# Kernel optimization log

Measured on AMD Instinct MI355X. Metric: run time of the kernel, lower is better.

## Reference

```python
import jax, jax.numpy as jnp
import numpy as np

B, S, DIM_IN, DIM_K, DIM_V = 4, 2048, 512, 2048, 64


def setup_inputs() -> dict:
    key = jax.random.key(0)
    k1, k2, k3, k4 = jax.random.split(key, 4)
    x = jax.random.normal(k1, (B, S, DIM_IN), dtype=jnp.float32)
    # nn.Linear(dim_in, d, bias=False) -> stored transposed here so y = x @ W
    Wq = jax.random.normal(k2, (DIM_IN, DIM_K), dtype=jnp.float32) / np.sqrt(DIM_IN)
    Wk = jax.random.normal(k3, (DIM_IN, DIM_K), dtype=jnp.float32) / np.sqrt(DIM_IN)
    Wv = jax.random.normal(k4, (DIM_IN, DIM_V), dtype=jnp.float32) / np.sqrt(DIM_IN)
    return {"x": x, "Wq": Wq, "Wk": Wk, "Wv": Wv}


def reference(x, Wq, Wk, Wv):
    dim_k = Wq.shape[-1]
    q = x @ Wq            # [B, S, dim_k]
    k = x @ Wk            # [B, S, dim_k]
    v = x @ Wv            # [B, S, dim_v]
    scores = jnp.einsum("bqd,bkd->bqk", q, k)  # [B, S, S]
    # causal mask: disallow attending to strictly-future positions
    seq = scores.shape[-1]
    mask = jnp.triu(jnp.ones((seq, seq), dtype=bool), k=1)
    scores = jnp.where(mask[None, :, :], -jnp.inf, scores)
    attn = jax.nn.softmax(scores / np.sqrt(dim_k).astype(np.float32), axis=-1)
    return attn @ v       # [B, S, dim_v]
```

## Files before the change

### kernel.cpp

```cpp
#include <hip/hip_runtime.h>
#include <hip/hip_bf16.h>
#include <math.h>

using bf16 = __hip_bfloat16;
typedef __bf16 bf16x8 __attribute__((ext_vector_type(8)));
typedef float floatx4 __attribute__((ext_vector_type(4)));

constexpr int BB = 4, SS = 2048, DIN = 512, DKK = 2048, DVV = 64;
constexpr int ROWS = BB * SS;
constexpr int LDY = 640;

constexpr size_t XB_OFF  = 0;
constexpr size_t WQB_OFF = XB_OFF  + 8388608;
constexpr size_t WKB_OFF = WQB_OFF + 2097152;
constexpr size_t WT2_OFF = WKB_OFF + 2097152;
constexpr size_t MTP_OFF = WT2_OFF + 655360;
constexpr size_t YV_OFF  = MTP_OFF + 8388608;
constexpr size_t VT_OFF  = YV_OFF  + 10485760;
constexpr size_t PRT_OFF = VT_OFF  + 1048576;
constexpr size_t STA_OFF = PRT_OFF + 16777216;

__device__ __forceinline__ void async_copy16(const bf16* g, const unsigned short* l) {
    __builtin_amdgcn_global_load_lds((const __attribute__((address_space(1))) void*)g,
                                     (__attribute__((address_space(3))) void*)l, 16, 0, 0);
}

__global__ __launch_bounds__(256) void prep(const float* __restrict__ x,
                                            const float* __restrict__ Wq,
                                            const float* __restrict__ Wk,
                                            const float* __restrict__ Wv,
                                            bf16* __restrict__ xb,
                                            bf16* __restrict__ wqb,
                                            bf16* __restrict__ wkb,
                                            bf16* __restrict__ wt2) {
    __shared__ float tile[32][33];
    const int bid = blockIdx.x;
    const int tid = threadIdx.x;

    if (bid < 4096) {
        int i = bid * 256 + tid;
        float4 v = reinterpret_cast<const float4*>(x)[i];
        union { bf16 h[4]; ushort4 u; } cv;
        cv.h[0] = __float2bfloat16(v.x);
        cv.h[1] = __float2bfloat16(v.y);
        cv.h[2] = __float2bfloat16(v.z);
        cv.h[3] = __float2bfloat16(v.w);
        reinterpret_cast<ushort4*>(xb)[i] = cv.u;
    } else if (bid < 6144) {
        int i = (bid - 4096) * 256 + tid;
        const float* src = (i < 262144) ? Wq : Wk;
        bf16* dst = (i < 262144) ? wqb : wkb;
        int j = (i < 262144) ? i : i - 262144;
        float4 v = reinterpret_cast<const float4*>(src)[j];
        union { bf16 h[4]; ushort4 u; } cv;
        cv.h[0] = __float2bfloat16(v.x);
        cv.h[1] = __float2bfloat16(v.y);
        cv.h[2] = __float2bfloat16(v.z);
        cv.h[3] = __float2bfloat16(v.w);
        reinterpret_cast<ushort4*>(dst)[j] = cv.u;
    } else {
        int idx = bid - 6144;
        int n0 = (idx & 1) * 32;
        int k0 = (idx >> 1) * 32;
        int nn = tid & 31, kk8 = tid >> 5;
        #pragma unroll
        for (int p = 0; p < 4; ++p) {
            int k = p * 8 + kk8;
            tile[k][nn] = Wv[(long long)(k0 + k) * 64 + n0 + nn];
        }
        __syncthreads();
        int kk = tid & 31, nn8 = tid >> 5;
        #pragma unroll
        for (int p = 0; p < 4; ++p) {
            int n = p * 8 + nn8;
            wt2[(long long)(512 + n0 + n) * 512 + k0 + kk] = __float2bfloat16(tile[kk][n]);
        }
    }
}

__global__ __launch_bounds__(256) void gemm_mt(const bf16* __restrict__ A,
                                               const bf16* __restrict__ Bt,
                                               float* __restrict__ Cp) {
    __shared__ __align__(16) unsigned short As[128 * 64];
    __shared__ __align__(16) unsigned short Bs[128 * 64];

    const int tid = threadIdx.x;
    const int lane = tid & 63, wave = tid >> 6;

    const int wg = (blockIdx.x & 7) * 16 + (blockIdx.x >> 3);
    const int z = wg >> 4;
    const int tile = wg & 15;
    const long long m0 = (long long)(tile >> 2) * 128;
    const long long n0 = (long long)(tile & 3) * 128;
    const int koff = z * 256;

    const int rIn = lane >> 3;
    const int cSwz = ((lane & 7) ^ rIn) * 8;
    const int wm0 = (wave >> 1) * 64, wn0 = (wave & 1) * 64;
    const int l15 = lane & 15, quad = lane >> 4;
    const int sw7 = l15 & 7;

    floatx4 acc[4][4] = {};

    for (int k0 = koff; k0 < koff + 256; k0 += 64) {
        #pragma unroll
        for (int t0 = 0; t0 < 8; ++t0) {
            int t = t0 * 4 + wave;
            if (t < 16)
                async_copy16(A + (m0 + t * 8 + rIn) * 2048LL + k0 + cSwz, &As[t * 512]);
            else
                async_copy16(Bt + (n0 + (t - 16) * 8 + rIn) * 2048LL + k0 + cSwz, &Bs[(t - 16) * 512]);
        }
        __syncthreads();
        #pragma unroll
        for (int sk = 0; sk < 2; ++sk) {
            const int rchunk = (((sk << 2) | quad) ^ sw7) * 8;
            bf16x8 af[4], bfr[4];
            #pragma unroll
            for (int mi = 0; mi < 4; ++mi)
                af[mi] = *reinterpret_cast<const bf16x8*>(&As[(wm0 + mi * 16 + l15) * 64 + rchunk]);
            #pragma unroll
            for (int ni = 0; ni < 4; ++ni)
                bfr[ni] = *reinterpret_cast<const bf16x8*>(&Bs[(wn0 + ni * 16 + l15) * 64 + rchunk]);
            #pragma unroll
            for (int mi = 0; mi < 4; ++mi)
                #pragma unroll
                for (int ni = 0; ni < 4; ++ni)
                    acc[mi][ni] = __builtin_amdgcn_mfma_f32_16x16x32_bf16(af[mi], bfr[ni],
                                                                          acc[mi][ni], 0, 0, 0);
        }
        __syncthreads();
    }

    float* C = Cp + (long long)z * 262144;
    #pragma unroll
    for (int mi = 0; mi < 4; ++mi) {
        long long row0 = m0 + wm0 + mi * 16 + quad * 4;
        #pragma unroll
        for (int ni = 0; ni < 4; ++ni) {
            long long col = n0 + wn0 + ni * 16 + l15;
            #pragma unroll
            for (int r = 0; r < 4; ++r)
                C[(row0 + r) * 512 + col] = acc[mi][ni][r];
        }
    }
}

__global__ __launch_bounds__(256) void reduce_mt(const float4* __restrict__ part,
                                                 bf16* __restrict__ wt2) {
    int i = blockIdx.x * 256 + threadIdx.x;
    float4 s = {0.f, 0.f, 0.f, 0.f};
    #pragma unroll
    for (int t = 0; t < 8; ++t) {
        float4 a = part[(long long)t * 65536 + i];
        s.x += a.x; s.y += a.y; s.z += a.z; s.w += a.w;
    }
    union { bf16 h[4]; ushort4 u; } cv;
    cv.h[0] = __float2bfloat16(s.x);
    cv.h[1] = __float2bfloat16(s.y);
    cv.h[2] = __float2bfloat16(s.z);
    cv.h[3] = __float2bfloat16(s.w);
    reinterpret_cast<ushort4*>(wt2)[i] = cv.u;
}

__global__ __launch_bounds__(256) void gemm_proj(const bf16* __restrict__ A,
                                                 const bf16* __restrict__ Bt,
                                                 bf16* __restrict__ C,
                                                 bf16* __restrict__ vt) {
    __shared__ __align__(16) unsigned short As[128 * 64];
    __shared__ __align__(16) unsigned short Bs[128 * 64];

    const int tid = threadIdx.x;
    const int lane = tid & 63, wave = tid >> 6;

    const int wg = (blockIdx.x & 7) * 40 + (blockIdx.x >> 3);
    const long long m0 = (long long)(wg / 5) * 128;
    const long long n0 = (long long)(wg % 5) * 128;

    const int rIn = lane >> 3;
    const int cSwz = ((lane & 7) ^ rIn) * 8;
    const int wm0 = (wave >> 1) * 64, wn0 = (wave & 1) * 64;
    const int l15 = lane & 15, quad = lane >> 4;
    const int sw7 = l15 & 7;

    floatx4 acc[4][4] = {};

    for (int k0 = 0; k0 < DIN; k0 += 64) {
        #pragma unroll
        for (int t0 = 0; t0 < 8; ++t0) {
            int t = t0 * 4 + wave;
            if (t < 16)
                async_copy16(A + (m0 + t * 8 + rIn) * (long long)DIN + k0 + cSwz, &As[t * 512]);
            else
                async_copy16(Bt + (n0 + (t - 16) * 8 + rIn) * (long long)DIN + k0 + cSwz, &Bs[(t - 16) * 512]);
        }
        __syncthreads();
        #pragma unroll
        for (int sk = 0; sk < 2; ++sk) {
            const int rchunk = (((sk << 2) | quad) ^ sw7) * 8;
            bf16x8 af[4], bfr[4];
            #pragma unroll
            for (int mi = 0; mi < 4; ++mi)
                af[mi] = *reinterpret_cast<const bf16x8*>(&As[(wm0 + mi * 16 + l15) * 64 + rchunk]);
            #pragma unroll
            for (int ni = 0; ni < 4; ++ni)
                bfr[ni] = *reinterpret_cast<const bf16x8*>(&Bs[(wn0 + ni * 16 + l15) * 64 + rchunk]);
            #pragma unroll
            for (int mi = 0; mi < 4; ++mi)
                #pragma unroll
                for (int ni = 0; ni < 4; ++ni)
                    acc[mi][ni] = __builtin_amdgcn_mfma_f32_16x16x32_bf16(af[mi], bfr[ni],
                                                                          acc[mi][ni], 0, 0, 0);
        }
        __syncthreads();
    }

    if (n0 < 512) {
        #pragma unroll
        for (int mi = 0; mi < 4; ++mi) {
            long long row0 = m0 + wm0 + mi * 16 + quad * 4;
            #pragma unroll
            for (int ni = 0; ni < 4; ++ni) {
                long long col = n0 + wn0 + ni * 16 + l15;
                #pragma unroll
                for (int r = 0; r < 4; ++r)
                    C[(row0 + r) * (long long)LDY + col] = __float2bfloat16(acc[mi][ni][r]);
            }
        }
    } else if (!(wave & 1)) {
        const int b = (int)(m0 >> 11);
        const int sbase = ((int)m0 & 2047) + wm0;
        #pragma unroll
        for (int mi = 0; mi < 4; ++mi) {
            int s0 = sbase + mi * 16 + quad * 4;
            #pragma unroll
            for (int ni = 0; ni < 4; ++ni) {
                int j = ni * 16 + l15;
                union { bf16 h[4]; ushort4 u; } cv;
                #pragma unroll
                for (int r = 0; r < 4; ++r)
                    cv.h[r] = __float2bfloat16(acc[mi][ni][r]);
                *reinterpret_cast<ushort4*>(vt + ((long long)(b * DVV + j)) * SS + s0) = cv.u;
            }
        }
    }
}

__global__ __launch_bounds__(512) void attn_fused(const bf16* __restrict__ yv,
                                                  const bf16* __restrict__ xb,
                                                  const bf16* __restrict__ vt,
                                                  bf16* __restrict__ part,
                                                  float* __restrict__ stats) {
    constexpr int BK = 64;
    constexpr float SCALE = 0.022097086912079608f;

    __shared__ __align__(16) char smem[37888];
    unsigned short* As = (unsigned short*)smem;
    unsigned short* Bs = (unsigned short*)(smem + 16384);
    unsigned short* Ps = (unsigned short*)smem;
    unsigned short* Vs = (unsigned short*)(smem + 18432);
    float* smax = (float*)(smem + 35840);
    float* ssum = (float*)(smem + 36864);

    const int wg = (blockIdx.x & 7) * 17 + (blockIdx.x >> 3);
    int by = (int)((sqrtf(8.f * (float)wg + 1.f) - 1.f) * 0.5f);
    while ((by + 1) * (by + 2) / 2 <= wg) ++by;
    while (by * (by + 1) / 2 > wg) --by;
    const int bx = wg - by * (by + 1) / 2;
    const int b = blockIdx.z;

    const bf16* A  = yv + (long long)b * SS * LDY;
    const bf16* Bt = xb + (long long)b * SS * 512;

    const int tid = threadIdx.x;
    const int lane = tid & 63, wave = tid >> 6;
    const long long m0 = (long long)by * 128;
    const long long n0 = (long long)bx * 128;

    const int rIn = lane >> 3;
    const int cSwz = ((lane & 7) ^ rIn) * 8;
    const int wm0 = (wave >> 1) * 32, wn0 = (wave & 1) * 64;
    const int l15 = lane & 15, quad = lane >> 4;
    const int sw7 = l15 & 7;

    floatx4 acc[2][4] = {};

    uint4 vreg[2];
    #pragma unroll
    for (int p = 0; p < 2; ++p) {
        int j = (tid >> 4) + p * 32;
        int ch = tid & 15;
        vreg[p] = *reinterpret_cast<const uint4*>(
            vt + ((long long)b * DVV + j) * SS + n0 + ch * 8);
    }

    auto issue = [&](int k0) {
        #pragma unroll
        for (int t0 = 0; t0 < 4; ++t0) {
            int t = t0 * 8 + wave;
            if (t < 16)
                async_copy16(A + (m0 + t * 8 + rIn) * (long long)LDY + k0 + cSwz,
                             &As[t * 512]);
            else
                async_copy16(Bt + (n0 + (t - 16) * 8 + rIn) * 512LL + k0 + cSwz,
                             &Bs[(t - 16) * 512]);
        }
    };

    for (int it = 0; it < DIN / BK; ++it) {
        issue(it * BK);
        __syncthreads();
        __builtin_amdgcn_s_setprio(1);
        #pragma unroll
        for (int sk = 0; sk < 2; ++sk) {
            const int rchunk = ((sk << 2) | quad) ^ sw7;
            bf16x8 af[2], bfr[4];
            #pragma unroll
            for (int mi = 0; mi < 2; ++mi)
                af[mi] = *reinterpret_cast<const bf16x8*>(
                    &As[(wm0 + mi * 16 + l15) * BK + rchunk * 8]);
            #pragma unroll
            for (int ni = 0; ni < 4; ++ni)
                bfr[ni] = *reinterpret_cast<const bf16x8*>(
                    &Bs[(wn0 + ni * 16 + l15) * BK + rchunk * 8]);
            #pragma unroll
            for (int mi = 0; mi < 2; ++mi)
                #pragma unroll
                for (int ni = 0; ni < 4; ++ni)
                    acc[mi][ni] = __builtin_amdgcn_mfma_f32_16x16x32_bf16(af[mi], bfr[ni],
                                                                          acc[mi][ni], 0, 0, 0);
        }
        __builtin_amdgcn_s_setprio(0);
        __syncthreads();
    }

    #pragma unroll
    for (int mi = 0; mi < 2; ++mi)
        #pragma unroll
        for (int ni = 0; ni < 4; ++ni)
            #pragma unroll
            for (int r = 0; r < 4; ++r) {
                float v = acc[mi][ni][r] * SCALE;
                if (bx == by) {
                    int row = wm0 + mi * 16 + quad * 4 + r;
                    int col = wn0 + ni * 16 + l15;
                    if (col > row) v = -INFINITY;
                }
                acc[mi][ni][r] = v;
            }

    float rmax[2][4];
    #pragma unroll
    for (int mi = 0; mi < 2; ++mi)
        #pragma unroll
        for (int r = 0; r < 4; ++r) {
            float m = fmaxf(fmaxf(acc[mi][0][r], acc[mi][1][r]),
                            fmaxf(acc[mi][2][r], acc[mi][3][r]));
            #pragma unroll
            for (int msk = 8; msk >= 1; msk >>= 1) m = fmaxf(m, __shfl_xor(m, msk));
            rmax[mi][r] = m;
            if (l15 == 0) smax[(wm0 + mi * 16 + quad * 4 + r) * 2 + (wave & 1)] = m;
        }
    __syncthreads();
    #pragma unroll
    for (int mi = 0; mi < 2; ++mi)
        #pragma unroll
        for (int r = 0; r < 4; ++r) {
            int row = wm0 + mi * 16 + quad * 4 + r;
            rmax[mi][r] = fmaxf(smax[row * 2], smax[row * 2 + 1]);
        }

    #pragma unroll
    for (int mi = 0; mi < 2; ++mi)
        #pragma unroll
        for (int r = 0; r < 4; ++r) {
            float s = 0.f;
            #pragma unroll
            for (int ni = 0; ni < 4; ++ni) {
                float p = __expf(acc[mi][ni][r] - rmax[mi][r]);
                acc[mi][ni][r] = p;
                s += p;
            }
            #pragma unroll
            for (int msk = 8; msk >= 1; msk >>= 1) s += __shfl_xor(s, msk);
            if (l15 == 0) ssum[(wm0 + mi * 16 + quad * 4 + r) * 2 + (wave & 1)] = s;
        }

    if ((wave & 1) == 0) {
        #pragma unroll
        for (int mi = 0; mi < 2; ++mi) {
            int row = wm0 + mi * 16 + quad * 4;
            #pragma unroll
            for (int ni = 0; ni < 4; ++ni) {
                int col = ni * 16 + l15;
                #pragma unroll
                for (int r = 0; r < 4; ++r)
                    Ps[(row + r) * 72 + col] =
                        (unsigned short)__bfloat16_as_ushort(__float2bfloat16(acc[mi][ni][r]));
            }
        }
    }
    #pragma unroll
    for (int p = 0; p < 2; ++p) {
        int j = (tid >> 4) + p * 32;
        int ch = tid & 15;
        *reinterpret_cast<uint4*>(&Vs[j * 136 + ((ch ^ (j & 7)) * 8)]) = vreg[p];
    }
    __syncthreads();

    if (tid < 128) {
        float m = fmaxf(smax[tid * 2], smax[tid * 2 + 1]);
        float l = ssum[tid * 2] + ssum[tid * 2 + 1];
        long long o = (((long long)b * 16 + bx) * SS + m0 + tid) * 2;
        stats[o] = m;
        stats[o + 1] = l;
    }

    const int wmv = wave * 16;
    floatx4 accO[4] = {};
    __builtin_amdgcn_s_setprio(1);
    #pragma unroll
    for (int sk = 0; sk < 2; ++sk) {
        bf16x8 af = *reinterpret_cast<const bf16x8*>(
            &Ps[(wmv + l15) * 72 + sk * 32 + quad * 8]);
        #pragma unroll
        for (int ni = 0; ni < 4; ++ni) {
            bf16x8 bfv = *reinterpret_cast<const bf16x8*>(
                &Vs[(ni * 16 + l15) * 136 + (((sk << 2) | quad) ^ sw7) * 8]);
            accO[ni] = __builtin_amdgcn_mfma_f32_16x16x32_bf16(af, bfv, accO[ni], 0, 0, 0);
        }
    }
    __builtin_amdgcn_s_setprio(0);
    __syncthreads();

    if ((wave & 1) == 1) {
        #pragma unroll
        for (int mi = 0; mi < 2; ++mi) {
            int row = wm0 + mi * 16 + quad * 4;
            #pragma unroll
            for (int ni = 0; ni < 4; ++ni) {
                int col = ni * 16 + l15;
                #pragma unroll
                for (int r = 0; r < 4; ++r)
                    Ps[(row + r) * 72 + col] =
                        (unsigned short)__bfloat16_as_ushort(__float2bfloat16(acc[mi][ni][r]));
            }
        }
    }
    __syncthreads();

    __builtin_amdgcn_s_setprio(1);
    #pragma unroll
    for (int sk = 0; sk < 2; ++sk) {
        const int kc = 2 + sk;
        bf16x8 af = *reinterpret_cast<const bf16x8*>(
            &Ps[(wmv + l15) * 72 + sk * 32 + quad * 8]);
        #pragma unroll
        for (int ni = 0; ni < 4; ++ni) {
            bf16x8 bfv = *reinterpret_cast<const bf16x8*>(
                &Vs[(ni * 16 + l15) * 136 + (((kc << 2) | quad) ^ sw7) * 8]);
            accO[ni] = __builtin_amdgcn_mfma_f32_16x16x32_bf16(af, bfv, accO[ni], 0, 0, 0);
        }
    }
    __builtin_amdgcn_s_setprio(0);

    #pragma unroll
    for (int ni = 0; ni < 4; ++ni)
        #pragma unroll
        for (int r = 0; r < 4; ++r)
            part[(((long long)b * 16 + bx) * SS + m0 + wmv + quad * 4 + r) * 64 + ni * 16 + l15]
                = __float2bfloat16(accO[ni][r]);
}

__global__ __launch_bounds__(256) void combine(const bf16* __restrict__ part,
                                               const float* __restrict__ stats,
                                               float* __restrict__ out) {
    int tid = blockIdx.x * 256 + threadIdx.x;
    int row = tid >> 3;
    int col8 = (tid & 7) * 8;
    int b = row >> 11, s = row & (SS - 1);
    int nt = (s >> 7) + 1;

    float m[16], l[16], M = -INFINITY;
    #pragma unroll
    for (int t = 0; t < 16; ++t)
        if (t < nt) {
            long long o = (((long long)b * 16 + t) * SS + s) * 2;
            m[t] = stats[o];
            l[t] = stats[o + 1];
            M = fmaxf(M, m[t]);
        }
    float O[8] = {};
    float L = 0.f;
    #pragma unroll
    for (int t = 0; t < 16; ++t)
        if (t < nt) {
            float wgt = __expf(m[t] - M);
            L += wgt * l[t];
            union { uint4 q; unsigned short u[8]; } ld;
            ld.q = *reinterpret_cast<const uint4*>(
                part + (((long long)b * 16 + t) * SS + s) * 64 + col8);
            #pragma unroll
            for (int j = 0; j < 8; ++j)
                O[j] += wgt * __uint_as_float((unsigned)ld.u[j] << 16);
        }
    float rinv = 1.0f / L;
    float4 o0 = {O[0] * rinv, O[1] * rinv, O[2] * rinv, O[3] * rinv};
    float4 o1 = {O[4] * rinv, O[5] * rinv, O[6] * rinv, O[7] * rinv};
    float4* dst = reinterpret_cast<float4*>(out + (long long)row * 64 + col8);
    dst[0] = o0;
    dst[1] = o1;
}

extern "C" void kernel_launch(void* const* d_in, const int* in_sizes, int n_in,
                              void* d_out, int out_size, void* d_ws, size_t ws_size,
                              hipStream_t stream) {
    const float* x  = (const float*)d_in[0];
    const float* Wq = (const float*)d_in[1];
    const float* Wk = (const float*)d_in[2];
    const float* Wv = (const float*)d_in[3];
    float* out = (float*)d_out;

    char* w = (char*)d_ws;
    bf16* xb   = (bf16*)(w + XB_OFF);
    bf16* wqb  = (bf16*)(w + WQB_OFF);
    bf16* wkb  = (bf16*)(w + WKB_OFF);
    bf16* wt2  = (bf16*)(w + WT2_OFF);
    float* mtp = (float*)(w + MTP_OFF);
    bf16* yv   = (bf16*)(w + YV_OFF);
    bf16* vt   = (bf16*)(w + VT_OFF);
    bf16* part = (bf16*)(w + PRT_OFF);
    float* stats = (float*)(w + STA_OFF);

    prep<<<6176, 256, 0, stream>>>(x, Wq, Wk, Wv, xb, wqb, wkb, wt2);

    gemm_mt<<<128, 256, 0, stream>>>(wkb, wqb, mtp);
    reduce_mt<<<65536 / 256, 256, 0, stream>>>((const float4*)mtp, wt2);

    gemm_proj<<<320, 256, 0, stream>>>(xb, wt2, yv, vt);

    attn_fused<<<dim3(136, 1, BB), 512, 0, stream>>>(yv, xb, vt, part, stats);

    combine<<<ROWS * 8 / 256, 256, 0, stream>>>(part, stats, out);
}
```

Before: 141.3 us.

## Enlarge fused attention tile to 256 query rows per workgroup

```diff
diff --git a/kernel.cpp b/kernel.cpp
--- a/kernel.cpp
+++ b/kernel.cpp
@@ -254,19 +254,18 @@
     constexpr int BK = 64;
     constexpr float SCALE = 0.022097086912079608f;
 
-    __shared__ __align__(16) char smem[37888];
+    __shared__ __align__(16) char smem[55296];
     unsigned short* As = (unsigned short*)smem;
-    unsigned short* Bs = (unsigned short*)(smem + 16384);
+    unsigned short* Bs = (unsigned short*)(smem + 32768);
     unsigned short* Ps = (unsigned short*)smem;
-    unsigned short* Vs = (unsigned short*)(smem + 18432);
-    float* smax = (float*)(smem + 35840);
-    float* ssum = (float*)(smem + 36864);
-
-    const int wg = (blockIdx.x & 7) * 17 + (blockIdx.x >> 3);
-    int by = (int)((sqrtf(8.f * (float)wg + 1.f) - 1.f) * 0.5f);
-    while ((by + 1) * (by + 2) / 2 <= wg) ++by;
-    while (by * (by + 1) / 2 > wg) --by;
-    const int bx = wg - by * (by + 1) / 2;
+    float* smax = (float*)(smem + 33792);
+    float* ssum = (float*)(smem + 35840);
+    unsigned short* Vs = (unsigned short*)(smem + 37888);
+
+    const int wg = (blockIdx.x & 7) * 9 + (blockIdx.x >> 3);
+    int by = 0;
+    while ((by + 1) * (by + 2) <= wg) ++by;
+    const int bx = wg - by * (by + 1);
     const int b = blockIdx.z;
 
     const bf16* A  = yv + (long long)b * SS * LDY;
@@ -274,16 +273,16 @@
 
     const int tid = threadIdx.x;
     const int lane = tid & 63, wave = tid >> 6;
-    const long long m0 = (long long)by * 128;
+    const long long m0 = (long long)by * 256;
     const long long n0 = (long long)bx * 128;
 
     const int rIn = lane >> 3;
     const int cSwz = ((lane & 7) ^ rIn) * 8;
-    const int wm0 = (wave >> 1) * 32, wn0 = (wave & 1) * 64;
+    const int wm0 = (wave >> 1) * 64, wn0 = (wave & 1) * 64;
     const int l15 = lane & 15, quad = lane >> 4;
     const int sw7 = l15 & 7;
 
-    floatx4 acc[2][4] = {};
+    floatx4 acc[4][4] = {};
 
     uint4 vreg[2];
     #pragma unroll
@@ -296,14 +295,14 @@
 
     auto issue = [&](int k0) {
         #pragma unroll
-        for (int t0 = 0; t0 < 4; ++t0) {
+        for (int t0 = 0; t0 < 6; ++t0) {
             int t = t0 * 8 + wave;
-            if (t < 16)
+            if (t < 32)
                 async_copy16(A + (m0 + t * 8 + rIn) * (long long)LDY + k0 + cSwz,
                              &As[t * 512]);
             else
-                async_copy16(Bt + (n0 + (t - 16) * 8 + rIn) * 512LL + k0 + cSwz,
-                             &Bs[(t - 16) * 512]);
+                async_copy16(Bt + (n0 + (t - 32) * 8 + rIn) * 512LL + k0 + cSwz,
+                             &Bs[(t - 32) * 512]);
         }
     };
 
@@ -313,18 +312,18 @@
         __builtin_amdgcn_s_setprio(1);
         #pragma unroll
         for (int sk = 0; sk < 2; ++sk) {
-            const int rchunk = ((sk << 2) | quad) ^ sw7;
-            bf16x8 af[2], bfr[4];
-            #pragma unroll
-            for (int mi = 0; mi < 2; ++mi)
+            const int rchunk = (((sk << 2) | quad) ^ sw7) * 8;
+            bf16x8 af[4], bfr[4];
+            #pragma unroll
+            for (int mi = 0; mi < 4; ++mi)
                 af[mi] = *reinterpret_cast<const bf16x8*>(
-                    &As[(wm0 + mi * 16 + l15) * BK + rchunk * 8]);
+                    &As[(wm0 + mi * 16 + l15) * BK + rchunk]);
             #pragma unroll
             for (int ni = 0; ni < 4; ++ni)
                 bfr[ni] = *reinterpret_cast<const bf16x8*>(
-                    &Bs[(wn0 + ni * 16 + l15) * BK + rchunk * 8]);
-            #pragma unroll
-            for (int mi = 0; mi < 2; ++mi)
+                    &Bs[(wn0 + ni * 16 + l15) * BK + rchunk]);
+            #pragma unroll
+            for (int mi = 0; mi < 4; ++mi)
                 #pragma unroll
                 for (int ni = 0; ni < 4; ++ni)
                     acc[mi][ni] = __builtin_amdgcn_mfma_f32_16x16x32_bf16(af[mi], bfr[ni],
@@ -334,24 +333,25 @@
         __syncthreads();
     }
 
-    #pragma unroll
-    for (int mi = 0; mi < 2; ++mi)
+    const bool diag = (bx >= 2 * by);
+    #pragma unroll
+    for (int mi = 0; mi < 4; ++mi)
         #pragma unroll
         for (int ni = 0; ni < 4; ++ni)
             #pragma unroll
             for (int r = 0; r < 4; ++r) {
                 float v = acc[mi][ni][r] * SCALE;
-                if (bx == by) {
-                    int row = wm0 + mi * 16 + quad * 4 + r;
-                    int col = wn0 + ni * 16 + l15;
-                    if (col > row) v = -INFINITY;
+                if (diag) {
+                    int grow = (int)m0 + wm0 + mi * 16 + quad * 4 + r;
+                    int gcol = (int)n0 + wn0 + ni * 16 + l15;
+                    if (gcol > grow) v = -INFINITY;
                 }
                 acc[mi][ni][r] = v;
             }
 
-    float rmax[2][4];
-    #pragma unroll
-    for (int mi = 0; mi < 2; ++mi)
+    float rmax[4][4];
+    #pragma unroll
+    for (int mi = 0; mi < 4; ++mi)
         #pragma unroll
         for (int r = 0; r < 4; ++r) {
             float m = fmaxf(fmaxf(acc[mi][0][r], acc[mi][1][r]),
@@ -363,7 +363,7 @@
         }
     __syncthreads();
     #pragma unroll
-    for (int mi = 0; mi < 2; ++mi)
+    for (int mi = 0; mi < 4; ++mi)
         #pragma unroll
         for (int r = 0; r < 4; ++r) {
             int row = wm0 + mi * 16 + quad * 4 + r;
@@ -371,7 +371,7 @@
         }
 
     #pragma unroll
-    for (int mi = 0; mi < 2; ++mi)
+    for (int mi = 0; mi < 4; ++mi)
         #pragma unroll
         for (int r = 0; r < 4; ++r) {
             float s = 0.f;
@@ -388,14 +388,14 @@
 
     if ((wave & 1) == 0) {
         #pragma unroll
-        for (int mi = 0; mi < 2; ++mi) {
+        for (int mi = 0; mi < 4; ++mi) {
             int row = wm0 + mi * 16 + quad * 4;
             #pragma unroll
             for (int ni = 0; ni < 4; ++ni) {
                 int col = ni * 16 + l15;
                 #pragma unroll
                 for (int r = 0; r < 4; ++r)
-                    Ps[(row + r) * 72 + col] =
+                    Ps[(row + r) * 66 + col] =
                         (unsigned short)__bfloat16_as_ushort(__float2bfloat16(acc[mi][ni][r]));
             }
         }
@@ -408,7 +408,7 @@
     }
     __syncthreads();
 
-    if (tid < 128) {
+    if (tid < 256) {
         float m = fmaxf(smax[tid * 2], smax[tid * 2 + 1]);
         float l = ssum[tid * 2] + ssum[tid * 2 + 1];
         long long o = (((long long)b * 16 + bx) * SS + m0 + tid) * 2;
@@ -416,18 +416,21 @@
         stats[o + 1] = l;
     }
 
-    const int wmv = wave * 16;
-    floatx4 accO[4] = {};
+    const int wmv = wave * 32;
+    floatx4 accO[2][4] = {};
     __builtin_amdgcn_s_setprio(1);
     #pragma unroll
     for (int sk = 0; sk < 2; ++sk) {
-        bf16x8 af = *reinterpret_cast<const bf16x8*>(
-            &Ps[(wmv + l15) * 72 + sk * 32 + quad * 8]);
-        #pragma unroll
-        for (int ni = 0; ni < 4; ++ni) {
-            bf16x8 bfv = *reinterpret_cast<const bf16x8*>(
-                &Vs[(ni * 16 + l15) * 136 + (((sk << 2) | quad) ^ sw7) * 8]);
-            accO[ni] = __builtin_amdgcn_mfma_f32_16x16x32_bf16(af, bfv, accO[ni], 0, 0, 0);
+        #pragma unroll
+        for (int mi = 0; mi < 2; ++mi) {
+            bf16x8 af = *reinterpret_cast<const bf16x8*>(
+                &Ps[(wmv + mi * 16 + l15) * 66 + sk * 32 + quad * 8]);
+            #pragma unroll
+            for (int ni = 0; ni < 4; ++ni) {
+                bf16x8 bfv = *reinterpret_cast<const bf16x8*>(
+                    &Vs[(ni * 16 + l15) * 136 + (((sk << 2) | quad) ^ sw7) * 8]);
+                accO[mi][ni] = __builtin_amdgcn_mfma_f32_16x16x32_bf16(af, bfv, accO[mi][ni], 0, 0, 0);
+            }
         }
     }
     __builtin_amdgcn_s_setprio(0);
@@ -435,14 +438,14 @@
 
     if ((wave & 1) == 1) {
         #pragma unroll
-        for (int mi = 0; mi < 2; ++mi) {
+        for (int mi = 0; mi < 4; ++mi) {
             int row = wm0 + mi * 16 + quad * 4;
             #pragma unroll
             for (int ni = 0; ni < 4; ++ni) {
                 int col = ni * 16 + l15;
                 #pragma unroll
                 for (int r = 0; r < 4; ++r)
-                    Ps[(row + r) * 72 + col] =
+                    Ps[(row + r) * 66 + col] =
                         (unsigned short)__bfloat16_as_ushort(__float2bfloat16(acc[mi][ni][r]));
             }
         }
@@ -453,23 +456,28 @@
     #pragma unroll
     for (int sk = 0; sk < 2; ++sk) {
         const int kc = 2 + sk;
-        bf16x8 af = *reinterpret_cast<const bf16x8*>(
-            &Ps[(wmv + l15) * 72 + sk * 32 + quad * 8]);
-        #pragma unroll
-        for (int ni = 0; ni < 4; ++ni) {
-            bf16x8 bfv = *reinterpret_cast<const bf16x8*>(
-                &Vs[(ni * 16 + l15) * 136 + (((kc << 2) | quad) ^ sw7) * 8]);
-            accO[ni] = __builtin_amdgcn_mfma_f32_16x16x32_bf16(af, bfv, accO[ni], 0, 0, 0);
+        #pragma unroll
+        for (int mi = 0; mi < 2; ++mi) {
+            bf16x8 af = *reinterpret_cast<const bf16x8*>(
+                &Ps[(wmv + mi * 16 + l15) * 66 + sk * 32 + quad * 8]);
+            #pragma unroll
+            for (int ni = 0; ni < 4; ++ni) {
+                bf16x8 bfv = *reinterpret_cast<const bf16x8*>(
+                    &Vs[(ni * 16 + l15) * 136 + (((kc << 2) | quad) ^ sw7) * 8]);
+                accO[mi][ni] = __builtin_amdgcn_mfma_f32_16x16x32_bf16(af, bfv, accO[mi][ni], 0, 0, 0);
+            }
         }
     }
     __builtin_amdgcn_s_setprio(0);
 
     #pragma unroll
-    for (int ni = 0; ni < 4; ++ni)
-        #pragma unroll
-        for (int r = 0; r < 4; ++r)
-            part[(((long long)b * 16 + bx) * SS + m0 + wmv + quad * 4 + r) * 64 + ni * 16 + l15]
-                = __float2bfloat16(accO[ni][r]);
+    for (int mi = 0; mi < 2; ++mi)
+        #pragma unroll
+        for (int ni = 0; ni < 4; ++ni)
+            #pragma unroll
+            for (int r = 0; r < 4; ++r)
+                part[(((long long)b * 16 + bx) * SS + m0 + wmv + mi * 16 + quad * 4 + r) * 64
+                     + ni * 16 + l15] = __float2bfloat16(accO[mi][ni][r]);
 }
 
 __global__ __launch_bounds__(256) void combine(const bf16* __restrict__ part,
@@ -539,7 +547,7 @@
 
     gemm_proj<<<320, 256, 0, stream>>>(xb, wt2, yv, vt);
 
-    attn_fused<<<dim3(136, 1, BB), 512, 0, stream>>>(yv, xb, vt, part, stats);
+    attn_fused<<<dim3(72, 1, BB), 512, 0, stream>>>(yv, xb, vt, part, stats);
 
     combine<<<ROWS * 8 / 256, 256, 0, stream>>>(part, stats, out);
 }
```

Result: slower. 171.0 us (+21.0%).

## Halve attention query tile to 64 rows with 256-thread blocks and more workgroups

Applied to the files above, without the earlier changes.

```diff
diff --git a/kernel.cpp b/kernel.cpp
--- a/kernel.cpp
+++ b/kernel.cpp
@@ -246,7 +246,7 @@
     }
 }
 
-__global__ __launch_bounds__(512) void attn_fused(const bf16* __restrict__ yv,
+__global__ __launch_bounds__(256) void attn_fused(const bf16* __restrict__ yv,
                                                   const bf16* __restrict__ xb,
                                                   const bf16* __restrict__ vt,
                                                   bf16* __restrict__ part,
@@ -254,19 +254,18 @@
     constexpr int BK = 64;
     constexpr float SCALE = 0.022097086912079608f;
 
-    __shared__ __align__(16) char smem[37888];
+    __shared__ __align__(16) char smem[24576];
     unsigned short* As = (unsigned short*)smem;
-    unsigned short* Bs = (unsigned short*)(smem + 16384);
+    unsigned short* Bs = (unsigned short*)(smem + 8192);
     unsigned short* Ps = (unsigned short*)smem;
-    unsigned short* Vs = (unsigned short*)(smem + 18432);
-    float* smax = (float*)(smem + 35840);
-    float* ssum = (float*)(smem + 36864);
-
-    const int wg = (blockIdx.x & 7) * 17 + (blockIdx.x >> 3);
-    int by = (int)((sqrtf(8.f * (float)wg + 1.f) - 1.f) * 0.5f);
-    while ((by + 1) * (by + 2) / 2 <= wg) ++by;
-    while (by * (by + 1) / 2 > wg) --by;
-    const int bx = wg - by * (by + 1) / 2;
+    unsigned short* Vs = (unsigned short*)(smem + 9216);
+    float* smax = (float*)(smem + 18432);
+    float* ssum = (float*)(smem + 18944);
+
+    const int wg = (blockIdx.x & 7) * 34 + (blockIdx.x >> 3);
+    int by = 0, c = 0;
+    while (c + (by >> 1) + 1 <= wg) { c += (by >> 1) + 1; ++by; }
+    const int bx = wg - c;
     const int b = blockIdx.z;
 
     const bf16* A  = yv + (long long)b * SS * LDY;
@@ -274,7 +273,7 @@
 
     const int tid = threadIdx.x;
     const int lane = tid & 63, wave = tid >> 6;
-    const long long m0 = (long long)by * 128;
+    const long long m0 = (long long)by * 64;
     const long long n0 = (long long)bx * 128;
 
     const int rIn = lane >> 3;
@@ -285,25 +284,26 @@
 
     floatx4 acc[2][4] = {};
 
-    uint4 vreg[2];
-    #pragma unroll
-    for (int p = 0; p < 2; ++p) {
-        int j = (tid >> 4) + p * 32;
-        int ch = tid & 15;
-        vreg[p] = *reinterpret_cast<const uint4*>(
-            vt + ((long long)b * DVV + j) * SS + n0 + ch * 8);
+    uint4 vreg[4];
+    {
+        int j = tid >> 2;
+        int ch = tid & 3;
+        #pragma unroll
+        for (int p = 0; p < 4; ++p)
+            vreg[p] = *reinterpret_cast<const uint4*>(
+                vt + ((long long)b * DVV + j) * SS + n0 + (ch + p * 4) * 8);
     }
 
     auto issue = [&](int k0) {
         #pragma unroll
-        for (int t0 = 0; t0 < 4; ++t0) {
-            int t = t0 * 8 + wave;
-            if (t < 16)
+        for (int t0 = 0; t0 < 6; ++t0) {
+            int t = t0 * 4 + wave;
+            if (t < 8)
                 async_copy16(A + (m0 + t * 8 + rIn) * (long long)LDY + k0 + cSwz,
                              &As[t * 512]);
             else
-                async_copy16(Bt + (n0 + (t - 16) * 8 + rIn) * 512LL + k0 + cSwz,
-                             &Bs[(t - 16) * 512]);
+                async_copy16(Bt + (n0 + (t - 8) * 8 + rIn) * 512LL + k0 + cSwz,
+                             &Bs[(t - 8) * 512]);
         }
     };
 
@@ -313,16 +313,16 @@
         __builtin_amdgcn_s_setprio(1);
         #pragma unroll
         for (int sk = 0; sk < 2; ++sk) {
-            const int rchunk = ((sk << 2) | quad) ^ sw7;
+            const int rchunk = (((sk << 2) | quad) ^ sw7) * 8;
             bf16x8 af[2], bfr[4];
             #pragma unroll
             for (int mi = 0; mi < 2; ++mi)
                 af[mi] = *reinterpret_cast<const bf16x8*>(
-                    &As[(wm0 + mi * 16 + l15) * BK + rchunk * 8]);
+                    &As[(wm0 + mi * 16 + l15) * BK + rchunk]);
             #pragma unroll
             for (int ni = 0; ni < 4; ++ni)
                 bfr[ni] = *reinterpret_cast<const bf16x8*>(
-                    &Bs[(wn0 + ni * 16 + l15) * BK + rchunk * 8]);
+                    &Bs[(wn0 + ni * 16 + l15) * BK + rchunk]);
             #pragma unroll
             for (int mi = 0; mi < 2; ++mi)
                 #pragma unroll
@@ -334,6 +334,7 @@
         __syncthreads();
     }
 
+    const bool diag = (n0 + 127 > m0);
     #pragma unroll
     for (int mi = 0; mi < 2; ++mi)
         #pragma unroll
@@ -341,10 +342,10 @@
             #pragma unroll
             for (int r = 0; r < 4; ++r) {
                 float v = acc[mi][ni][r] * SCALE;
-                if (bx == by) {
-                    int row = wm0 + mi * 16 + quad * 4 + r;
-                    int col = wn0 + ni * 16 + l15;
-                    if (col > row) v = -INFINITY;
+                if (diag) {
+                    int grow = (int)m0 + wm0 + mi * 16 + quad * 4 + r;
+                    int gcol = (int)n0 + wn0 + ni * 16 + l15;
+                    if (gcol > grow) v = -INFINITY;
                 }
                 acc[mi][ni][r] = v;
             }
@@ -400,15 +401,18 @@
             }
         }
     }
-    #pragma unroll
-    for (int p = 0; p < 2; ++p) {
-        int j = (tid >> 4) + p * 32;
-        int ch = tid & 15;
-        *reinterpret_cast<uint4*>(&Vs[j * 136 + ((ch ^ (j & 7)) * 8)]) = vreg[p];
+    {
+        int j = tid >> 2;
+        int ch = tid & 3;
+        #pragma unroll
+        for (int pp = 0; pp < 2; ++pp) {
+            int chh = ch + pp * 4;
+            *reinterpret_cast<uint4*>(&Vs[j * 72 + ((chh ^ (j & 7)) * 8)]) = vreg[pp];
+        }
     }
     __syncthreads();
 
-    if (tid < 128) {
+    if (tid < 64) {
         float m = fmaxf(smax[tid * 2], smax[tid * 2 + 1]);
         float l = ssum[tid * 2] + ssum[tid * 2 + 1];
         long long o = (((long long)b * 16 + bx) * SS + m0 + tid) * 2;
@@ -426,7 +430,7 @@
         #pragma unroll
         for (int ni = 0; ni < 4; ++ni) {
             bf16x8 bfv = *reinterpret_cast<const bf16x8*>(
-                &Vs[(ni * 16 + l15) * 136 + (((sk << 2) | quad) ^ sw7) * 8]);
+                &Vs[(ni * 16 + l15) * 72 + ((((sk << 2) | quad)) ^ sw7) * 8]);
             accO[ni] = __builtin_amdgcn_mfma_f32_16x16x32_bf16(af, bfv, accO[ni], 0, 0, 0);
         }
     }
@@ -447,18 +451,26 @@
             }
         }
     }
+    {
+        int j = tid >> 2;
+        int ch = tid & 3;
+        #pragma unroll
+        for (int pp = 0; pp < 2; ++pp) {
+            int chh = ch + pp * 4;
+            *reinterpret_cast<uint4*>(&Vs[j * 72 + ((chh ^ (j & 7)) * 8)]) = vreg[2 + pp];
+        }
+    }
     __syncthreads();
 
     __builtin_amdgcn_s_setprio(1);
     #pragma unroll
     for (int sk = 0; sk < 2; ++sk) {
-        const int kc = 2 + sk;
         bf16x8 af = *reinterpret_cast<const bf16x8*>(
             &Ps[(wmv + l15) * 72 + sk * 32 + quad * 8]);
         #pragma unroll
         for (int ni = 0; ni < 4; ++ni) {
             bf16x8 bfv = *reinterpret_cast<const bf16x8*>(
-                &Vs[(ni * 16 + l15) * 136 + (((kc << 2) | quad) ^ sw7) * 8]);
+                &Vs[(ni * 16 + l15) * 72 + ((((sk << 2) | quad)) ^ sw7) * 8]);
             accO[ni] = __builtin_amdgcn_mfma_f32_16x16x32_bf16(af, bfv, accO[ni], 0, 0, 0);
         }
     }
@@ -539,7 +551,7 @@
 
     gemm_proj<<<320, 256, 0, stream>>>(xb, wt2, yv, vt);
 
-    attn_fused<<<dim3(136, 1, BB), 512, 0, stream>>>(yv, xb, vt, part, stats);
+    attn_fused<<<dim3(272, 1, BB), 256, 0, stream>>>(yv, xb, vt, part, stats);
 
     combine<<<ROWS * 8 / 256, 256, 0, stream>>>(part, stats, out);
 }
```

New measurement: 140.4 us. No clear change (-0.7%).
